# Kernel tuning notes

Hardware: AMD Instinct MI355X
Metric: run time of the kernel (lower is better)

The kernel has to match this reference:

```python
import jax, jax.numpy as jnp
import numpy as np

B, S, D, H = 2, 2048, 1024, 16
DK = D // H


def setup_inputs() -> dict:
    key = jax.random.key(0)
    ks = jax.random.split(key, 11)
    s = 1.0 / np.sqrt(D)
    return {
        "q": jax.random.normal(ks[0], (B, S, D), jnp.float32),
        "k": jax.random.normal(ks[1], (B, S, D), jnp.float32),
        "v": jax.random.normal(ks[2], (B, S, D), jnp.float32),
        "mask": jnp.ones((B, 1, S, S), jnp.int32),
        "Wq": jax.random.normal(ks[3], (D, D), jnp.float32) * s,
        "bq": jnp.zeros((D,), jnp.float32),
        "Wk": jax.random.normal(ks[4], (D, D), jnp.float32) * s,
        "bk": jnp.zeros((D,), jnp.float32),
        "Wv": jax.random.normal(ks[5], (D, D), jnp.float32) * s,
        "bv": jnp.zeros((D,), jnp.float32),
        "Wo": jax.random.normal(ks[6], (D, D), jnp.float32) * s,
        "bo": jnp.zeros((D,), jnp.float32),
    }


def reference(q, k, v, mask, Wq, bq, Wk, bk, Wv, bv, Wo, bo):
    # Note: original torch code calls non-in-place masked_fill and discards the
    # result, so the mask has no mathematical effect; we preserve that.
    qh = (q @ Wq + bq).reshape(B, S, H, DK).transpose(0, 2, 1, 3)  # [B,H,S,DK]
    kh = (k @ Wk + bk).reshape(B, S, H, DK).transpose(0, 2, 1, 3)
    vh = (v @ Wv + bv).reshape(B, S, H, DK).transpose(0, 2, 1, 3)
    scores = jnp.einsum("bhqd,bhkd->bhqk", qh, kh) / jnp.sqrt(jnp.float32(DK))
    attn = jax.nn.softmax(scores, axis=-1)
    out = jnp.einsum("bhqk,bhkd->bhqd", attn, vh)  # [B,H,S,DK]
    out = out.transpose(0, 2, 1, 3).reshape(B, S, D)
    return out @ Wo + bo
```

## Files before the change

kernel.cpp:

```cpp
#include <hip/hip_runtime.h>

#define S_LEN    2048
#define D_MODEL  1024
#define N_HEADS  16
#define HEAD_DIM 64
#define BATCH    2

typedef __bf16 bf16x8 __attribute__((ext_vector_type(8)));
typedef float  floatx4 __attribute__((ext_vector_type(4)));
typedef float  floatx16 __attribute__((ext_vector_type(16)));

__device__ __forceinline__ unsigned short f2bf(float f) {
    union { float f; unsigned int u; } v;
    v.f = f;
    unsigned int u = v.u;
    u += 0x7fffu + ((u >> 16) & 1u);
    return (unsigned short)(u >> 16);
}

__device__ __forceinline__ unsigned int pk_rne(float a, float b) {
    union { float f; unsigned int u; } ua, ub;
    ua.f = a; ub.f = b;
    unsigned int x = ua.u + 0x7fffu + ((ua.u >> 16) & 1u);
    unsigned int y = ub.u + 0x7fffu + ((ub.u >> 16) & 1u);
    return __builtin_amdgcn_perm(y, x, 0x07060302);
}

__device__ __forceinline__ void gload_lds16(const unsigned short* g, unsigned short* l) {
    __builtin_amdgcn_global_load_lds(
        (const __attribute__((address_space(1))) void*)(const void*)g,
        (__attribute__((address_space(3))) void*)(void*)l,
        16, 0, 0);
}

#define LDS_FENCE() __asm__ volatile("s_waitcnt lgkmcnt(0)" ::: "memory")

struct PrepArgs {
    const float* src[3]; unsigned short* dst[3];
    const float* W[4];   unsigned short* Wt[4];
};

#define CONV_BLOCKS (3 * 4096)

__global__ void prep_kernel(PrepArgs args) {
    const int bid = blockIdx.x;
    if (bid < CONV_BLOCKS) {
        const int t   = bid >> 12;
        const int blk = bid & 4095;
        const int i   = blk * 256 + threadIdx.x;
        float4 f = reinterpret_cast<const float4*>(args.src[t])[i];
        ushort4 o;
        o.x = f2bf(f.x); o.y = f2bf(f.y); o.z = f2bf(f.z); o.w = f2bf(f.w);
        reinterpret_cast<ushort4*>(args.dst[t])[i] = o;
    } else {
        __shared__ unsigned short tile[64][65];
        const int r  = bid - CONV_BLOCKS;
        const int w  = r >> 8;
        const int xy = r & 255;
        const int n0 = (xy & 15) * 64, k0 = (xy >> 4) * 64;
        const float* W = args.W[w];
        unsigned short* Wt = args.Wt[w];
        for (int rep = 0; rep < 16; ++rep) {
            int e = rep * 256 + threadIdx.x;
            int kk = e >> 6, nn = e & 63;
            tile[kk][nn] = f2bf(W[(size_t)(k0 + kk) * D_MODEL + n0 + nn]);
        }
        __syncthreads();
        for (int rep = 0; rep < 16; ++rep) {
            int e = rep * 256 + threadIdx.x;
            int nn = e >> 6, kk = e & 63;
            Wt[(size_t)(n0 + nn) * D_MODEL + k0 + kk] = tile[kk][nn];
        }
    }
}

template <int TM, int TN, int MODE>
__device__ __forceinline__
void gemm_body(const unsigned short* __restrict__ A,
               const unsigned short* __restrict__ Bt,
               const float* __restrict__ bias,
               void* __restrict__ out,
               int m0, int n0, float scale,
               unsigned short* smem) {
    constexpr int MT = TM / 32;
    constexpr int NT = TN / 32;
    unsigned short* As = smem;
    unsigned short* Bs = smem + TM * 32;
    const int tid  = threadIdx.x;
    const int wid  = tid >> 6;
    const int lane = tid & 63;

    floatx4 acc[MT][NT];
#pragma unroll
    for (int i = 0; i < MT; ++i)
#pragma unroll
        for (int j = 0; j < NT; ++j) acc[i][j] = (floatx4)0.0f;

    const int srow = lane >> 2;
    const int gch  = (lane & 3) ^ ((srow >> 1) & 3);
    const int wr = (wid >> 1) * (TM / 2);
    const int wc = (wid & 1) * (TN / 2);
    const int fr = lane & 15;
    const int fq = lane >> 4;
    const int swz = (fq ^ ((fr >> 1) & 3)) * 8;

    for (int k0 = 0; k0 < D_MODEL; k0 += 32) {
        if (k0) __syncthreads();
#pragma unroll
        for (int ci = 0; ci < (TM + TN) / 64; ++ci) {
            const int c = wid + ci * 4;
            if (c < TM / 16) {
                const int row = c * 16 + srow;
                gload_lds16(A + (size_t)(m0 + row) * D_MODEL + k0 + gch * 8, As + c * 512);
            } else {
                const int cb = c - TM / 16;
                const int row = cb * 16 + srow;
                gload_lds16(Bt + (size_t)(n0 + row) * D_MODEL + k0 + gch * 8, Bs + cb * 512);
            }
        }
        __syncthreads();

        bf16x8 af[MT], bfv[NT];
#pragma unroll
        for (int t = 0; t < MT; ++t)
            af[t] = *reinterpret_cast<const bf16x8*>(As + (wr + t * 16 + fr) * 32 + swz);
#pragma unroll
        for (int t = 0; t < NT; ++t)
            bfv[t] = *reinterpret_cast<const bf16x8*>(Bs + (wc + t * 16 + fr) * 32 + swz);
#pragma unroll
        for (int mt = 0; mt < MT; ++mt)
#pragma unroll
            for (int nt = 0; nt < NT; ++nt) {
                if (MODE == 1)
                    acc[mt][nt] = __builtin_amdgcn_mfma_f32_16x16x32_bf16(af[mt], bfv[nt], acc[mt][nt], 0, 0, 0);
                else
                    acc[mt][nt] = __builtin_amdgcn_mfma_f32_16x16x32_bf16(bfv[nt], af[mt], acc[mt][nt], 0, 0, 0);
            }
    }

    __syncthreads();

    if (MODE == 0) {
        unsigned short* rp = smem + wid * 1024;
        unsigned short* outbf = (unsigned short*)out;
        float4 b4[NT];
#pragma unroll
        for (int nt = 0; nt < NT; ++nt)
            b4[nt] = *reinterpret_cast<const float4*>(bias + n0 + wc + nt * 16 + fq * 4);
        const int hh = (n0 + wc) >> 6;
#pragma unroll
        for (int mt = 0; mt < MT; ++mt) {
#pragma unroll
            for (int nt = 0; nt < NT; ++nt) {
                const float* bb = reinterpret_cast<const float*>(&b4[nt]);
#pragma unroll
                for (int p = 0; p < 2; ++p) {
                    float v0 = (acc[mt][nt][2 * p]     + bb[2 * p])     * scale;
                    float v1 = (acc[mt][nt][2 * p + 1] + bb[2 * p + 1]) * scale;
                    *reinterpret_cast<unsigned int*>(rp + fr * 64 + nt * 16 + fq * 4 + 2 * p) = pk_rne(v0, v1);
                }
            }
            LDS_FENCE();
#pragma unroll
            for (int j = 0; j < 2; ++j) {
                const int row = (lane >> 3) + j * 8;
                const int m = m0 + wr + mt * 16 + row;
                const int b = m >> 11, s = m & (S_LEN - 1);
                uint4 val = *reinterpret_cast<const uint4*>(rp + row * 64 + (lane & 7) * 8);
                *reinterpret_cast<uint4*>(outbf + (((size_t)(b * N_HEADS + hh) * S_LEN + s) * HEAD_DIM) + (lane & 7) * 8) = val;
            }
            LDS_FENCE();
        }
    } else if (MODE == 1) {
        unsigned short* rp = smem + wid * 1024;
        unsigned short* outbf = (unsigned short*)out;
        float bval[NT];
#pragma unroll
        for (int nt = 0; nt < NT; ++nt) bval[nt] = bias[n0 + wc + nt * 16 + fr];
#pragma unroll
        for (int nt = 0; nt < NT; ++nt) {
#pragma unroll
            for (int mt = 0; mt < MT; ++mt) {
#pragma unroll
                for (int p = 0; p < 2; ++p) {
                    float v0 = acc[mt][nt][2 * p]     + bval[nt];
                    float v1 = acc[mt][nt][2 * p + 1] + bval[nt];
                    *reinterpret_cast<unsigned int*>(rp + fr * 64 + mt * 16 + fq * 4 + 2 * p) = pk_rne(v0, v1);
                }
            }
            LDS_FENCE();
#pragma unroll
            for (int j = 0; j < 2; ++j) {
                const int row = (lane >> 3) + j * 8;
                const int n = n0 + wc + nt * 16 + row;
                const int h = n >> 6, dk = n & 63;
                const int mch = m0 + wr + (lane & 7) * 8;
                const int b = mch >> 11, s = mch & (S_LEN - 1);
                uint4 val = *reinterpret_cast<const uint4*>(rp + row * 64 + (lane & 7) * 8);
                *reinterpret_cast<uint4*>(outbf + ((size_t)(b * N_HEADS + h) * HEAD_DIM + dk) * S_LEN + s) = val;
            }
            LDS_FENCE();
        }
    } else {
        float* rpf = reinterpret_cast<float*>(smem) + wid * 1024;
        float* outf = (float*)out;
        float4 b4[NT];
#pragma unroll
        for (int nt = 0; nt < NT; ++nt)
            b4[nt] = *reinterpret_cast<const float4*>(bias + n0 + wc + nt * 16 + fq * 4);
#pragma unroll
        for (int mt = 0; mt < MT; ++mt) {
#pragma unroll
            for (int nt = 0; nt < NT; ++nt) {
                const float* bb = reinterpret_cast<const float*>(&b4[nt]);
#pragma unroll
                for (int p = 0; p < 2; ++p) {
                    float2 w;
                    w.x = acc[mt][nt][2 * p]     + bb[2 * p];
                    w.y = acc[mt][nt][2 * p + 1] + bb[2 * p + 1];
                    *reinterpret_cast<float2*>(rpf + fr * 64 + nt * 16 + fq * 4 + 2 * p) = w;
                }
            }
            LDS_FENCE();
#pragma unroll
            for (int j = 0; j < 4; ++j) {
                const int row = (lane >> 4) + j * 4;
                const int m = m0 + wr + mt * 16 + row;
                float4 val = *reinterpret_cast<const float4*>(rpf + row * 64 + (lane & 15) * 4);
                *reinterpret_cast<float4*>(outf + (size_t)m * D_MODEL + n0 + wc + (lane & 15) * 4) = val;
            }
            LDS_FENCE();
        }
    }
}

struct QKVArgs {
    const unsigned short* A[3];
    const unsigned short* Bt[3];
    const float* bias[3];
    unsigned short* out[3];
};

__global__ __launch_bounds__(256)
void qkv_gemm_kernel(QKVArgs args) {
    __shared__ __align__(16) unsigned short smem[8192];
    const int z = blockIdx.z;
    const int m0 = blockIdx.y * 128;
    const int n0 = blockIdx.x * 128;
    if (z == 0)
        gemm_body<128, 128, 0>(args.A[0], args.Bt[0], args.bias[0], args.out[0], m0, n0, 0.18033688011112f, smem);
    else if (z == 1)
        gemm_body<128, 128, 0>(args.A[1], args.Bt[1], args.bias[1], args.out[1], m0, n0, 1.0f, smem);
    else
        gemm_body<128, 128, 1>(args.A[2], args.Bt[2], args.bias[2], args.out[2], m0, n0, 1.0f, smem);
}

__global__ __launch_bounds__(256)
void oproj_gemm_kernel(const unsigned short* __restrict__ A,
                       const unsigned short* __restrict__ Bt,
                       const float* __restrict__ bias,
                       float* __restrict__ out) {
    __shared__ __align__(16) unsigned short smem[8192];
    gemm_body<64, 128, 2>(A, Bt, bias, out, blockIdx.y * 64, blockIdx.x * 128, 1.0f, smem);
}

__global__ __launch_bounds__(256)
void attn_kernel(const unsigned short* __restrict__ qhp,
                 const unsigned short* __restrict__ khp,
                 const unsigned short* __restrict__ vtp,
                 unsigned short* __restrict__ outp) {
    __shared__ __align__(16) unsigned short Ks[128 * 64];
    __shared__ __align__(16) unsigned short Vs[64 * 128];

    const int tid  = threadIdx.x;
    const int wid  = tid >> 6;
    const int lane = tid & 63;
    const int b = blockIdx.z, h = blockIdx.y;
    const int q0 = blockIdx.x * 128;
    const int q31  = lane & 31;
    const int half = lane >> 5;

    const unsigned short* qbase = qhp + (size_t)(b * N_HEADS + h) * S_LEN * HEAD_DIM;
    const unsigned short* kbase = khp + (size_t)(b * N_HEADS + h) * S_LEN * HEAD_DIM;
    const unsigned short* vbase = vtp + (size_t)(b * N_HEADS + h) * HEAD_DIM * S_LEN;

    bf16x8 qf[4];
#pragma unroll
    for (int kc = 0; kc < 4; ++kc)
        qf[kc] = *reinterpret_cast<const bf16x8*>(
            qbase + (size_t)(q0 + wid * 32 + q31) * HEAD_DIM + kc * 16 + half * 8);

    floatx16 o_acc[2];
    o_acc[0] = (floatx16)0.0f; o_acc[1] = (floatx16)0.0f;
    float l_part = 0.0f;

    const int srow  = lane >> 3;
    const int gch   = (lane & 7) ^ srow;
    const int srow4 = lane >> 4;

    for (int it = 0; it < S_LEN / 128; ++it) {
        const int kv0 = it * 128;
        __syncthreads();
#pragma unroll
        for (int i = 0; i < 4; ++i) {
            const int c = wid * 4 + i;
            const int krow = c * 8 + srow;
            gload_lds16(kbase + (size_t)(kv0 + krow) * HEAD_DIM + gch * 8, Ks + c * 512);
            const int vrow = c * 4 + srow4;
            const int gchv = (lane & 15) ^ (vrow & 7);
            gload_lds16(vbase + (size_t)vrow * S_LEN + kv0 + gchv * 8, Vs + c * 512);
        }
        __syncthreads();

#pragma unroll
        for (int mt = 0; mt < 4; ++mt) {
            const int krow = mt * 32 + q31;
            const int ksw  = krow & 7;
            floatx16 st = (floatx16)0.0f;
#pragma unroll
            for (int kc = 0; kc < 4; ++kc) {
                bf16x8 kf = *reinterpret_cast<const bf16x8*>(
                    Ks + krow * 64 + (((kc * 2 + half) ^ ksw) * 8));
                st = __builtin_amdgcn_mfma_f32_32x32x16_bf16(kf, qf[kc], st, 0, 0, 0);
            }

            float p[16];
#pragma unroll
            for (int r = 0; r < 16; ++r) p[r] = __builtin_amdgcn_exp2f(st[r]);
#pragma unroll
            for (int r = 0; r < 16; r += 4)
                l_part += (p[r] + p[r + 1]) + (p[r + 2] + p[r + 3]);

            unsigned int u[8], x[8];
#pragma unroll
            for (int g = 0; g < 8; ++g) u[g] = pk_rne(p[2 * g], p[2 * g + 1]);
#pragma unroll
            for (int g = 0; g < 8; ++g) x[g] = (unsigned int)__shfl_xor((int)u[g], 32);

#pragma unroll
            for (int c = 0; c < 2; ++c) {
                uint4 pd;
                pd.x = half ? x[4 * c + 2] : u[4 * c];
                pd.y = half ? x[4 * c + 3] : u[4 * c + 1];
                pd.z = half ? u[4 * c + 2] : x[4 * c];
                pd.w = half ? u[4 * c + 3] : x[4 * c + 1];
                union { uint4 i; bf16x8 v; } pf; pf.i = pd;
                const int cg = mt * 2 + c;
#pragma unroll
                for (int dm = 0; dm < 2; ++dm) {
                    const int drow = dm * 32 + q31;
                    bf16x8 vf = *reinterpret_cast<const bf16x8*>(
                        Vs + drow * 128 + (((cg * 2 + half) ^ (drow & 7)) * 8));
                    o_acc[dm] = __builtin_amdgcn_mfma_f32_32x32x16_bf16(vf, pf.v, o_acc[dm], 0, 0, 0);
                }
            }
        }
    }

    const float l = l_part + __shfl_xor(l_part, 32);
    const float linv = __builtin_amdgcn_rcpf(l);

    const int q = q0 + wid * 32 + q31;
    unsigned short* orow = outp + ((size_t)(b * S_LEN + q)) * D_MODEL + h * HEAD_DIM;
#pragma unroll
    for (int dm = 0; dm < 2; ++dm)
#pragma unroll
        for (int g = 0; g < 8; ++g) {
            const int d = dm * 32 + 8 * (g >> 1) + 2 * (g & 1) + 4 * half;
            *reinterpret_cast<unsigned int*>(orow + d) =
                pk_rne(o_acc[dm][2 * g] * linv, o_acc[dm][2 * g + 1] * linv);
        }
}

extern "C" void kernel_launch(void* const* d_in, const int* in_sizes, int n_in,
                              void* d_out, int out_size, void* d_ws, size_t ws_size,
                              hipStream_t stream) {
    (void)in_sizes; (void)n_in; (void)out_size; (void)ws_size;
    const float* q  = (const float*)d_in[0];
    const float* k  = (const float*)d_in[1];
    const float* v  = (const float*)d_in[2];
    const float* Wq = (const float*)d_in[4];
    const float* bq = (const float*)d_in[5];
    const float* Wk = (const float*)d_in[6];
    const float* bk = (const float*)d_in[7];
    const float* Wv = (const float*)d_in[8];
    const float* bv = (const float*)d_in[9];
    const float* Wo = (const float*)d_in[10];
    const float* bo = (const float*)d_in[11];
    float* out = (float*)d_out;

    char* ws = (char*)d_ws;
    const size_t SZ_ACT = (size_t)BATCH * S_LEN * D_MODEL * 2;
    const size_t SZ_W   = (size_t)D_MODEL * D_MODEL * 2;
    unsigned short* qb   = (unsigned short*)(ws);
    unsigned short* kb   = (unsigned short*)(ws + SZ_ACT);
    unsigned short* vb   = (unsigned short*)(ws + 2 * SZ_ACT);
    unsigned short* Wqt  = (unsigned short*)(ws + 3 * SZ_ACT);
    unsigned short* Wkt  = (unsigned short*)(ws + 3 * SZ_ACT + SZ_W);
    unsigned short* Wvt  = (unsigned short*)(ws + 3 * SZ_ACT + 2 * SZ_W);
    unsigned short* Wot  = (unsigned short*)(ws + 3 * SZ_ACT + 3 * SZ_W);
    unsigned short* qhb  = (unsigned short*)(ws + 3 * SZ_ACT + 4 * SZ_W);
    unsigned short* khb  = (unsigned short*)(ws + 4 * SZ_ACT + 4 * SZ_W);
    unsigned short* vtb  = (unsigned short*)(ws + 5 * SZ_ACT + 4 * SZ_W);
    unsigned short* attn = qb;

    PrepArgs pargs;
    pargs.src[0] = q;  pargs.src[1] = k;  pargs.src[2] = v;
    pargs.dst[0] = qb; pargs.dst[1] = kb; pargs.dst[2] = vb;
    pargs.W[0] = Wq;  pargs.W[1] = Wk;  pargs.W[2] = Wv;  pargs.W[3] = Wo;
    pargs.Wt[0] = Wqt; pargs.Wt[1] = Wkt; pargs.Wt[2] = Wvt; pargs.Wt[3] = Wot;
    prep_kernel<<<dim3(CONV_BLOCKS + 1024), 256, 0, stream>>>(pargs);

    QKVArgs gargs;
    gargs.A[0] = qb;  gargs.A[1] = kb;  gargs.A[2] = vb;
    gargs.Bt[0] = Wqt; gargs.Bt[1] = Wkt; gargs.Bt[2] = Wvt;
    gargs.bias[0] = bq; gargs.bias[1] = bk; gargs.bias[2] = bv;
    gargs.out[0] = qhb; gargs.out[1] = khb; gargs.out[2] = vtb;
    qkv_gemm_kernel<<<dim3(8, 32, 3), 256, 0, stream>>>(gargs);

    attn_kernel<<<dim3(S_LEN / 128, N_HEADS, BATCH), 256, 0, stream>>>(qhb, khb, vtb, attn);

    oproj_gemm_kernel<<<dim3(8, 64), 256, 0, stream>>>(attn, Wot, bo, out);
}
```

Baseline: 259.7 us.

## Split attention over KV halves and merge partials inside output projection GEMM

```diff
diff --git a/kernel.cpp b/kernel.cpp
--- a/kernel.cpp
+++ b/kernel.cpp
@@ -24,6 +24,12 @@
     unsigned int x = ua.u + 0x7fffu + ((ua.u >> 16) & 1u);
     unsigned int y = ub.u + 0x7fffu + ((ub.u >> 16) & 1u);
     return __builtin_amdgcn_perm(y, x, 0x07060302);
+}
+
+__device__ __forceinline__ unsigned int pk_tr(float a, float b) {
+    union { float f; unsigned int u; } ua, ub;
+    ua.f = a; ub.f = b;
+    return __builtin_amdgcn_perm(ub.u, ua.u, 0x07060302);
 }
 
 __device__ __forceinline__ void gload_lds16(const unsigned short* g, unsigned short* l) {
@@ -171,7 +177,7 @@
             }
             LDS_FENCE();
         }
-    } else if (MODE == 1) {
+    } else {
         unsigned short* rp = smem + wid * 1024;
         unsigned short* outbf = (unsigned short*)out;
         float bval[NT];
@@ -198,36 +204,6 @@
                 const int b = mch >> 11, s = mch & (S_LEN - 1);
                 uint4 val = *reinterpret_cast<const uint4*>(rp + row * 64 + (lane & 7) * 8);
                 *reinterpret_cast<uint4*>(outbf + ((size_t)(b * N_HEADS + h) * HEAD_DIM + dk) * S_LEN + s) = val;
-            }
-            LDS_FENCE();
-        }
-    } else {
-        float* rpf = reinterpret_cast<float*>(smem) + wid * 1024;
-        float* outf = (float*)out;
-        float4 b4[NT];
-#pragma unroll
-        for (int nt = 0; nt < NT; ++nt)
-            b4[nt] = *reinterpret_cast<const float4*>(bias + n0 + wc + nt * 16 + fq * 4);
-#pragma unroll
-        for (int mt = 0; mt < MT; ++mt) {
-#pragma unroll
-            for (int nt = 0; nt < NT; ++nt) {
-                const float* bb = reinterpret_cast<const float*>(&b4[nt]);
-#pragma unroll
-                for (int p = 0; p < 2; ++p) {
-                    float2 w;
-                    w.x = acc[mt][nt][2 * p]     + bb[2 * p];
-                    w.y = acc[mt][nt][2 * p + 1] + bb[2 * p + 1];
-                    *reinterpret_cast<float2*>(rpf + fr * 64 + nt * 16 + fq * 4 + 2 * p) = w;
-                }
-            }
-            LDS_FENCE();
-#pragma unroll
-            for (int j = 0; j < 4; ++j) {
-                const int row = (lane >> 4) + j * 4;
-                const int m = m0 + wr + mt * 16 + row;
-                float4 val = *reinterpret_cast<const float4*>(rpf + row * 64 + (lane & 15) * 4);
-                *reinterpret_cast<float4*>(outf + (size_t)m * D_MODEL + n0 + wc + (lane & 15) * 4) = val;
             }
             LDS_FENCE();
         }
@@ -256,26 +232,155 @@
 }
 
 __global__ __launch_bounds__(256)
-void oproj_gemm_kernel(const unsigned short* __restrict__ A,
-                       const unsigned short* __restrict__ Bt,
+void oproj_gemm_kernel(const float* __restrict__ Opart,
+                       const float* __restrict__ lbuf,
+                       const unsigned short* __restrict__ Wot,
                        const float* __restrict__ bias,
                        float* __restrict__ out) {
-    __shared__ __align__(16) unsigned short smem[8192];
-    gemm_body<64, 128, 2>(A, Bt, bias, out, blockIdx.y * 64, blockIdx.x * 128, 1.0f, smem);
-}
-
-__global__ __launch_bounds__(256)
+    __shared__ __align__(16) unsigned short smem[12288];
+
+    const int tid  = threadIdx.x;
+    const int wid  = tid >> 6;
+    const int lane = tid & 63;
+    const int m0 = blockIdx.y * 64;
+    const int n0 = blockIdx.x * 128;
+
+    const int arow = tid & 63;
+    const int afq  = tid >> 6;
+    const int am   = m0 + arow;
+    const float* a0p = Opart + (size_t)am * D_MODEL + afq * 8;
+    const float* a1p = Opart + 4194304 + (size_t)am * D_MODEL + afq * 8;
+    const int aoff = arow * 32 + ((afq ^ ((arow >> 1) & 3)) * 8);
+
+    const int srow = lane >> 2;
+    const int gch  = (lane & 3) ^ ((srow >> 1) & 3);
+
+    const int wr = (wid >> 1) * 32;
+    const int wc = (wid & 1) * 64;
+    const int fr = lane & 15;
+    const int fq = lane >> 4;
+    const int swz = (fq ^ ((fr >> 1) & 3)) * 8;
+
+    floatx4 acc[2][4];
+#pragma unroll
+    for (int i = 0; i < 2; ++i)
+#pragma unroll
+        for (int j = 0; j < 4; ++j) acc[i][j] = (floatx4)0.0f;
+
+    float4 ra0 = *reinterpret_cast<const float4*>(a0p);
+    float4 ra1 = *reinterpret_cast<const float4*>(a0p + 4);
+    float4 rb0 = *reinterpret_cast<const float4*>(a1p);
+    float4 rb1 = *reinterpret_cast<const float4*>(a1p + 4);
+    float  rlv = lbuf[(size_t)am * 16] + lbuf[65536 + (size_t)am * 16];
+#pragma unroll
+    for (int ci = 0; ci < 2; ++ci) {
+        const int cb = wid + ci * 4;
+        const int row = cb * 16 + srow;
+        gload_lds16(Wot + (size_t)(n0 + row) * D_MODEL + gch * 8, smem + 4096 + cb * 512);
+    }
+    {
+        const float linv = __builtin_amdgcn_rcpf(rlv);
+        uint4 u;
+        u.x = pk_rne((ra0.x + rb0.x) * linv, (ra0.y + rb0.y) * linv);
+        u.y = pk_rne((ra0.z + rb0.z) * linv, (ra0.w + rb0.w) * linv);
+        u.z = pk_rne((ra1.x + rb1.x) * linv, (ra1.y + rb1.y) * linv);
+        u.w = pk_rne((ra1.z + rb1.z) * linv, (ra1.w + rb1.w) * linv);
+        *reinterpret_cast<uint4*>(smem + aoff) = u;
+    }
+    __syncthreads();
+
+    for (int k0 = 0; k0 < D_MODEL; k0 += 32) {
+        const int buf = (k0 >> 5) & 1;
+        unsigned short* Asb = smem + buf * 2048;
+        unsigned short* Bsb = smem + 4096 + buf * 4096;
+        unsigned short* Asn = smem + (buf ^ 1) * 2048;
+        unsigned short* Bsn = smem + 4096 + (buf ^ 1) * 4096;
+        const bool more = (k0 + 32) < D_MODEL;
+        if (more) {
+            const int k1 = k0 + 32;
+            ra0 = *reinterpret_cast<const float4*>(a0p + k1);
+            ra1 = *reinterpret_cast<const float4*>(a0p + k1 + 4);
+            rb0 = *reinterpret_cast<const float4*>(a1p + k1);
+            rb1 = *reinterpret_cast<const float4*>(a1p + k1 + 4);
+            rlv = lbuf[(size_t)am * 16 + (k1 >> 6)] + lbuf[65536 + (size_t)am * 16 + (k1 >> 6)];
+#pragma unroll
+            for (int ci = 0; ci < 2; ++ci) {
+                const int cb = wid + ci * 4;
+                const int row = cb * 16 + srow;
+                gload_lds16(Wot + (size_t)(n0 + row) * D_MODEL + k1 + gch * 8, Bsn + cb * 512);
+            }
+        }
+
+        bf16x8 af[2], bfv[4];
+#pragma unroll
+        for (int t = 0; t < 2; ++t)
+            af[t] = *reinterpret_cast<const bf16x8*>(Asb + (wr + t * 16 + fr) * 32 + swz);
+#pragma unroll
+        for (int t = 0; t < 4; ++t)
+            bfv[t] = *reinterpret_cast<const bf16x8*>(Bsb + (wc + t * 16 + fr) * 32 + swz);
+#pragma unroll
+        for (int mt = 0; mt < 2; ++mt)
+#pragma unroll
+            for (int nt = 0; nt < 4; ++nt)
+                acc[mt][nt] = __builtin_amdgcn_mfma_f32_16x16x32_bf16(bfv[nt], af[mt], acc[mt][nt], 0, 0, 0);
+
+        if (more) {
+            const float linv = __builtin_amdgcn_rcpf(rlv);
+            uint4 u;
+            u.x = pk_rne((ra0.x + rb0.x) * linv, (ra0.y + rb0.y) * linv);
+            u.y = pk_rne((ra0.z + rb0.z) * linv, (ra0.w + rb0.w) * linv);
+            u.z = pk_rne((ra1.x + rb1.x) * linv, (ra1.y + rb1.y) * linv);
+            u.w = pk_rne((ra1.z + rb1.z) * linv, (ra1.w + rb1.w) * linv);
+            *reinterpret_cast<uint4*>(Asn + aoff) = u;
+        }
+        __syncthreads();
+    }
+
+    float* rpf = reinterpret_cast<float*>(smem) + wid * 1024;
+    float4 b4[4];
+#pragma unroll
+    for (int nt = 0; nt < 4; ++nt)
+        b4[nt] = *reinterpret_cast<const float4*>(bias + n0 + wc + nt * 16 + fq * 4);
+#pragma unroll
+    for (int mt = 0; mt < 2; ++mt) {
+#pragma unroll
+        for (int nt = 0; nt < 4; ++nt) {
+            const float* bb = reinterpret_cast<const float*>(&b4[nt]);
+#pragma unroll
+            for (int p = 0; p < 2; ++p) {
+                float2 w;
+                w.x = acc[mt][nt][2 * p]     + bb[2 * p];
+                w.y = acc[mt][nt][2 * p + 1] + bb[2 * p + 1];
+                *reinterpret_cast<float2*>(rpf + fr * 64 + nt * 16 + fq * 4 + 2 * p) = w;
+            }
+        }
+        LDS_FENCE();
+#pragma unroll
+        for (int j = 0; j < 4; ++j) {
+            const int row = (lane >> 4) + j * 4;
+            const int m = m0 + wr + mt * 16 + row;
+            float4 val = *reinterpret_cast<const float4*>(rpf + row * 64 + (lane & 15) * 4);
+            *reinterpret_cast<float4*>(out + (size_t)m * D_MODEL + n0 + wc + (lane & 15) * 4) = val;
+        }
+        LDS_FENCE();
+    }
+}
+
+__global__ __launch_bounds__(256, 4)
 void attn_kernel(const unsigned short* __restrict__ qhp,
                  const unsigned short* __restrict__ khp,
                  const unsigned short* __restrict__ vtp,
-                 unsigned short* __restrict__ outp) {
+                 float* __restrict__ opart,
+                 float* __restrict__ lbuf) {
     __shared__ __align__(16) unsigned short Ks[128 * 64];
     __shared__ __align__(16) unsigned short Vs[64 * 128];
 
     const int tid  = threadIdx.x;
     const int wid  = tid >> 6;
     const int lane = tid & 63;
-    const int b = blockIdx.z, h = blockIdx.y;
+    const int z = blockIdx.z;
+    const int b = z >> 1, split = z & 1;
+    const int h = blockIdx.y;
     const int q0 = blockIdx.x * 128;
     const int q31  = lane & 31;
     const int half = lane >> 5;
@@ -290,16 +395,20 @@
         qf[kc] = *reinterpret_cast<const bf16x8*>(
             qbase + (size_t)(q0 + wid * 32 + q31) * HEAD_DIM + kc * 16 + half * 8);
 
+    bf16x8 ones;
+#pragma unroll
+    for (int i = 0; i < 8; ++i) ones[i] = (__bf16)1.0f;
+
     floatx16 o_acc[2];
     o_acc[0] = (floatx16)0.0f; o_acc[1] = (floatx16)0.0f;
-    float l_part = 0.0f;
+    floatx16 l_acc = (floatx16)0.0f;
 
     const int srow  = lane >> 3;
     const int gch   = (lane & 7) ^ srow;
     const int srow4 = lane >> 4;
 
-    for (int it = 0; it < S_LEN / 128; ++it) {
-        const int kv0 = it * 128;
+    for (int ii = 0; ii < 8; ++ii) {
+        const int kv0 = (split * 8 + ii) * 128;
         __syncthreads();
 #pragma unroll
         for (int i = 0; i < 4; ++i) {
@@ -327,13 +436,10 @@
             float p[16];
 #pragma unroll
             for (int r = 0; r < 16; ++r) p[r] = __builtin_amdgcn_exp2f(st[r]);
-#pragma unroll
-            for (int r = 0; r < 16; r += 4)
-                l_part += (p[r] + p[r + 1]) + (p[r + 2] + p[r + 3]);
 
             unsigned int u[8], x[8];
 #pragma unroll
-            for (int g = 0; g < 8; ++g) u[g] = pk_rne(p[2 * g], p[2 * g + 1]);
+            for (int g = 0; g < 8; ++g) u[g] = pk_tr(p[2 * g], p[2 * g + 1]);
 #pragma unroll
             for (int g = 0; g < 8; ++g) x[g] = (unsigned int)__shfl_xor((int)u[g], 32);
 
@@ -346,6 +452,7 @@
                 pd.w = half ? u[4 * c + 3] : x[4 * c + 1];
                 union { uint4 i; bf16x8 v; } pf; pf.i = pd;
                 const int cg = mt * 2 + c;
+                l_acc = __builtin_amdgcn_mfma_f32_32x32x16_bf16(ones, pf.v, l_acc, 0, 0, 0);
 #pragma unroll
                 for (int dm = 0; dm < 2; ++dm) {
                     const int drow = dm * 32 + q31;
@@ -357,19 +464,20 @@
         }
     }
 
-    const float l = l_part + __shfl_xor(l_part, 32);
-    const float linv = __builtin_amdgcn_rcpf(l);
-
     const int q = q0 + wid * 32 + q31;
-    unsigned short* orow = outp + ((size_t)(b * S_LEN + q)) * D_MODEL + h * HEAD_DIM;
+    const size_t m = (size_t)b * S_LEN + q;
+    float* obase = opart + (size_t)split * 4194304 + m * D_MODEL + h * HEAD_DIM;
 #pragma unroll
     for (int dm = 0; dm < 2; ++dm)
 #pragma unroll
         for (int g = 0; g < 8; ++g) {
             const int d = dm * 32 + 8 * (g >> 1) + 2 * (g & 1) + 4 * half;
-            *reinterpret_cast<unsigned int*>(orow + d) =
-                pk_rne(o_acc[dm][2 * g] * linv, o_acc[dm][2 * g + 1] * linv);
-        }
+            float2 w;
+            w.x = o_acc[dm][2 * g];
+            w.y = o_acc[dm][2 * g + 1];
+            *reinterpret_cast<float2*>(obase + d) = w;
+        }
+    if (!half) lbuf[(size_t)split * 65536 + m * 16 + h] = l_acc[0];
 }
 
 extern "C" void kernel_launch(void* const* d_in, const int* in_sizes, int n_in,
@@ -390,19 +498,19 @@
     float* out = (float*)d_out;
 
     char* ws = (char*)d_ws;
-    const size_t SZ_ACT = (size_t)BATCH * S_LEN * D_MODEL * 2;
-    const size_t SZ_W   = (size_t)D_MODEL * D_MODEL * 2;
+    const size_t MB = 1024 * 1024;
     unsigned short* qb   = (unsigned short*)(ws);
-    unsigned short* kb   = (unsigned short*)(ws + SZ_ACT);
-    unsigned short* vb   = (unsigned short*)(ws + 2 * SZ_ACT);
-    unsigned short* Wqt  = (unsigned short*)(ws + 3 * SZ_ACT);
-    unsigned short* Wkt  = (unsigned short*)(ws + 3 * SZ_ACT + SZ_W);
-    unsigned short* Wvt  = (unsigned short*)(ws + 3 * SZ_ACT + 2 * SZ_W);
-    unsigned short* Wot  = (unsigned short*)(ws + 3 * SZ_ACT + 3 * SZ_W);
-    unsigned short* qhb  = (unsigned short*)(ws + 3 * SZ_ACT + 4 * SZ_W);
-    unsigned short* khb  = (unsigned short*)(ws + 4 * SZ_ACT + 4 * SZ_W);
-    unsigned short* vtb  = (unsigned short*)(ws + 5 * SZ_ACT + 4 * SZ_W);
-    unsigned short* attn = qb;
+    unsigned short* kb   = (unsigned short*)(ws + 8 * MB);
+    unsigned short* vb   = (unsigned short*)(ws + 16 * MB);
+    unsigned short* Wqt  = (unsigned short*)(ws + 24 * MB);
+    unsigned short* Wkt  = (unsigned short*)(ws + 26 * MB);
+    unsigned short* Wvt  = (unsigned short*)(ws + 28 * MB);
+    unsigned short* Wot  = (unsigned short*)(ws + 32 * MB);
+    unsigned short* qhb  = (unsigned short*)(ws + 34 * MB);
+    unsigned short* khb  = (unsigned short*)(ws + 42 * MB);
+    unsigned short* vtb  = (unsigned short*)(ws + 50 * MB);
+    float*          opart = (float*)(ws);
+    float*          lbuf  = (float*)(ws + 58 * MB);
 
     PrepArgs pargs;
     pargs.src[0] = q;  pargs.src[1] = k;  pargs.src[2] = v;
@@ -418,7 +526,7 @@
     gargs.out[0] = qhb; gargs.out[1] = khb; gargs.out[2] = vtb;
     qkv_gemm_kernel<<<dim3(8, 32, 3), 256, 0, stream>>>(gargs);
 
-    attn_kernel<<<dim3(S_LEN / 128, N_HEADS, BATCH), 256, 0, stream>>>(qhb, khb, vtb, attn);
-
-    oproj_gemm_kernel<<<dim3(8, 64), 256, 0, stream>>>(attn, Wot, bo, out);
-}
+    attn_kernel<<<dim3(S_LEN / 128, N_HEADS, BATCH * 2), 256, 0, stream>>>(qhb, khb, vtb, opart, lbuf);
+
+    oproj_gemm_kernel<<<dim3(8, 64), 256, 0, stream>>>(opart, lbuf, Wot, bo, out);
+}
```

After: 300.6 us. 1.16x slower.
